# Kernel tuning notes

Measured on AMD Instinct MI355X. Metric: run time of the kernel, lower is better.

The kernel has to match this reference:

```python
import jax, jax.numpy as jnp
import numpy as np

N_NODES = 100000
N_EDGES = 1600000
D = 128
N_GRAPHS = 128
N_LAYERS = 3


def setup_inputs() -> dict:
    key = jax.random.key(0)
    ks = jax.random.split(key, 3 + 4 * N_LAYERS)
    x = jax.random.normal(ks[0], (N_NODES, D), dtype=jnp.float32)
    edge_index = jax.random.randint(ks[1], (2, N_EDGES), 0, N_NODES, dtype=jnp.int64)
    batch = jnp.sort(jax.random.randint(ks[2], (N_NODES,), 0, N_GRAPHS, dtype=jnp.int64))
    inp = {"x": x, "edge_index": edge_index, "batch": batch}
    scale = 1.0 / np.sqrt(D)
    for l in range(N_LAYERS):
        inp[f"W1_{l}"] = jax.random.normal(ks[3 + 4 * l], (D, D), dtype=jnp.float32) * scale
        inp[f"b1_{l}"] = jnp.zeros((D,), dtype=jnp.float32)
        inp[f"W2_{l}"] = jax.random.normal(ks[4 + 4 * l], (D, D), dtype=jnp.float32) * scale
        inp[f"b2_{l}"] = jnp.zeros((D,), dtype=jnp.float32)
    return inp


def _gin_conv(x, edge_index, W1, b1, W2, b2):
    # GINConv with eps=0: out = MLP(x + sum_{j in N(i)} x_j)
    msgs = x[edge_index[0]]                                   # [E, D] gather
    agg = jax.ops.segment_sum(msgs, edge_index[1], num_segments=N_NODES)
    h = x + agg
    h = jax.nn.relu(h @ W1 + b1)
    return h @ W2 + b2


def reference(x, edge_index, batch,
              W1_0, b1_0, W2_0, b2_0,
              W1_1, b1_1, W2_1, b2_1,
              W1_2, b1_2, W2_2, b2_2):
    params = [(W1_0, b1_0, W2_0, b2_0), (W1_1, b1_1, W2_1, b2_1), (W1_2, b1_2, W2_2, b2_2)]
    h = x
    for l in range(N_LAYERS - 1):
        h = _gin_conv(h, edge_index, *params[l])
        h = jax.nn.relu(h)  # act; dropout with drop_ratio=0 is identity
    node_emb = _gin_conv(h, edge_index, *params[-1])  # JK='last'
    # global_mean_pool
    sums = jax.ops.segment_sum(node_emb, batch, num_segments=N_GRAPHS)
    counts = jax.ops.segment_sum(jnp.ones((N_NODES, 1), node_emb.dtype), batch, num_segments=N_GRAPHS)
    graph_emb = sums / jnp.maximum(counts, 1.0)
    return graph_emb
```

## Files before the change

kernel.cpp:

```cpp
#include <hip/hip_runtime.h>
#include <hip/hip_bf16.h>

#define N_NODES 100000
#define N_PAD   100032
#define N_EDGES 1600000
#define DIM 128
#define N_GRAPHS 128
#define NBKT 98
#define BSTRIDE 18432
#define TILES (N_PAD / 16)
#define GRID_FUSED 1563
#define POOL_BLKS ((N_NODES + 127) / 128)
#define B1_BATCH 4096
#define B1_GRID ((N_EDGES + B1_BATCH - 1) / B1_BATCH)

typedef unsigned short u16;
typedef unsigned int u32;
typedef __attribute__((ext_vector_type(8))) short bf16x8;
typedef __attribute__((ext_vector_type(8))) unsigned short u16x8;
typedef __attribute__((ext_vector_type(4))) float f32x4;

#define MFMA(A, B, C) __builtin_amdgcn_mfma_f32_16x16x32_bf16(A, B, C, 0, 0, 0)

__device__ __forceinline__ u16 f2bf(float x) {
    u32 u = __float_as_uint(x);
    u = (u + 0x7FFFu + ((u >> 16) & 1u)) >> 16;
    return (u16)u;
}
__device__ __forceinline__ float bf2f(u16 u) {
    return __uint_as_float(((u32)u) << 16);
}

__global__ __launch_bounds__(256) void bucket1_kernel(const int* __restrict__ src,
                                                      const int* __restrict__ dst,
                                                      u32* __restrict__ cursorB,
                                                      u32* __restrict__ pairs) {
    __shared__ int lh[NBKT];
    __shared__ u32 lbase[NBKT];
    int t = threadIdx.x;
    if (t < NBKT) lh[t] = 0;
    __syncthreads();
    int e0 = blockIdx.x * B1_BATCH;
    int d[16], s[16], rk[16];
#pragma unroll
    for (int k = 0; k < 16; ++k) {
        int e = e0 + t + k * 256;
        if (e < N_EDGES) {
            d[k] = dst[e];
            s[k] = src[e];
            rk[k] = atomicAdd(&lh[d[k] >> 10], 1);
        }
    }
    __syncthreads();
    if (t < NBKT) lbase[t] = atomicAdd(&cursorB[t], (u32)lh[t]) + (u32)(t * BSTRIDE);
    __syncthreads();
#pragma unroll
    for (int k = 0; k < 16; ++k) {
        int e = e0 + t + k * 256;
        if (e < N_EDGES) {
            u32 pos = lbase[d[k] >> 10] + (u32)rk[k];
            pairs[pos] = ((u32)(d[k] & 1023) << 22) | (u32)s[k];
        }
    }
}

__global__ __launch_bounds__(1024) void bucket2_kernel(const u32* __restrict__ cursorB,
                                                       const u32* __restrict__ pairs,
                                                       int* __restrict__ row_ptr,
                                                       int* __restrict__ csr) {
    __shared__ int lh[1024];
    __shared__ int rc[1024];
    __shared__ int bs[128];
    int b = blockIdx.x, t = threadIdx.x;

    if (t < 128) bs[t] = (t < NBKT) ? (int)cursorB[t] : 0;
    __syncthreads();
    for (int off = 1; off < 128; off <<= 1) {
        int v = (t < 128 && t >= off) ? bs[t - off] : 0;
        __syncthreads();
        if (t < 128) bs[t] += v;
        __syncthreads();
    }
    int cnt = (int)cursorB[b];
    int bbase = (b == 0) ? 0 : bs[b - 1];

    lh[t] = 0;
    __syncthreads();
    const u32* pb = pairs + (size_t)b * BSTRIDE;
    for (int i = t; i < cnt; i += 1024) atomicAdd(&lh[__builtin_nontemporal_load(pb + i) >> 22], 1);
    __syncthreads();

    int own = lh[t];
    for (int off = 1; off < 1024; off <<= 1) {
        int v = (t >= off) ? lh[t - off] : 0;
        __syncthreads();
        lh[t] += v;
        __syncthreads();
    }
    int excl = lh[t] - own;
    int node = b * 1024 + t;
    if (node < N_NODES) row_ptr[node] = bbase + excl;
    if (b == 0 && t == 0) row_ptr[N_NODES] = N_EDGES;
    rc[t] = bbase + excl;
    __syncthreads();

    for (int i = t; i < cnt; i += 1024) {
        u32 p = __builtin_nontemporal_load(pb + i);
        int pos = atomicAdd(&rc[p >> 22], 1);
        csr[pos] = (int)(p & 0x3FFFFFu);
    }
}

__global__ __launch_bounds__(256) void xprep_kernel(const float* __restrict__ x,
                                                    u16* __restrict__ hb) {
    int i = blockIdx.x * 256 + threadIdx.x;
    if (i < N_NODES * 32) {
        float4 v = ((const float4*)x)[i];
        ushort4 o;
        o.x = f2bf(v.x); o.y = f2bf(v.y); o.z = f2bf(v.z); o.w = f2bf(v.w);
        ((ushort4*)hb)[i] = o;
    }
}

struct WPrepArgs {
    const float* w[6];
    u16* buf[6];
};
__global__ __launch_bounds__(256) void wprep_kernel(WPrepArgs p) {
    int m = blockIdx.y;
    int idx = blockIdx.x * 256 + threadIdx.x;
    int n = idx >> 7, k = idx & 127;
    float v = p.w[m][k * 128 + n];
    u16 hi = f2bf(v);
    p.buf[m][idx] = hi;
    p.buf[m][idx + 16384] = f2bf(v - bf2f(hi));
}

#define HS 136
__global__ __launch_bounds__(256, 2) void gin_layer(const u16* __restrict__ hin,
                                                    const int* __restrict__ rp,
                                                    const int* __restrict__ csr,
                                                    const u16* __restrict__ W1,
                                                    const float* __restrict__ b1,
                                                    const u16* __restrict__ W2,
                                                    const float* __restrict__ b2,
                                                    u16* __restrict__ hout, int relu) {
    __shared__ u16 Hh[64 * HS];
    __shared__ u16 Hl[64 * HS];
    int tid = threadIdx.x;
    int lane = tid & 63, wave = tid >> 6;
    int m16 = lane & 15, quad = lane >> 4;
    int colBase = wave * 32;
    int t0 = blockIdx.x * 4;
    int r0 = t0 * 16;

    {
        int qw = tid >> 4;
        int f  = tid & 15;
        int nb = r0 + qw * 4;
        const u16x8* h8 = (const u16x8*)hin;
#pragma unroll
        for (int j = 0; j < 4; ++j) {
            int n = nb + j;
            int nl = qw * 4 + j;
            float a[8];
            if (n < N_NODES) {
                u16x8 sv = h8[(size_t)n * 16 + f];
#pragma unroll
                for (int r = 0; r < 8; ++r) a[r] = bf2f(sv[r]);
                int s = rp[n], e = rp[n + 1];
                int i = s;
                for (; i + 8 <= e; i += 8) {
                    u16x8 v0 = h8[(size_t)csr[i + 0] * 16 + f];
                    u16x8 v1 = h8[(size_t)csr[i + 1] * 16 + f];
                    u16x8 v2 = h8[(size_t)csr[i + 2] * 16 + f];
                    u16x8 v3 = h8[(size_t)csr[i + 3] * 16 + f];
                    u16x8 v4 = h8[(size_t)csr[i + 4] * 16 + f];
                    u16x8 v5 = h8[(size_t)csr[i + 5] * 16 + f];
                    u16x8 v6 = h8[(size_t)csr[i + 6] * 16 + f];
                    u16x8 v7 = h8[(size_t)csr[i + 7] * 16 + f];
#pragma unroll
                    for (int r = 0; r < 8; ++r)
                        a[r] += ((bf2f(v0[r]) + bf2f(v1[r])) + (bf2f(v2[r]) + bf2f(v3[r]))) +
                                ((bf2f(v4[r]) + bf2f(v5[r])) + (bf2f(v6[r]) + bf2f(v7[r])));
                }
                for (; i < e; ++i) {
                    u16x8 v = h8[(size_t)csr[i] * 16 + f];
#pragma unroll
                    for (int r = 0; r < 8; ++r) a[r] += bf2f(v[r]);
                }
            } else {
#pragma unroll
                for (int r = 0; r < 8; ++r) a[r] = 0.f;
            }
            u16x8 o;
#pragma unroll
            for (int r = 0; r < 8; ++r) o[r] = f2bf(a[r]);
            *(u16x8*)&Hh[nl * HS + f * 8] = o;
        }
    }
    __syncthreads();

    bf16x8 aH[4][4];
#pragma unroll
    for (int p = 0; p < 4; ++p)
#pragma unroll
        for (int kb = 0; kb < 4; ++kb)
            aH[p][kb] = *(const bf16x8*)&Hh[(p * 16 + m16) * HS + kb * 32 + quad * 8];
    __syncthreads();

    float b1v[2][4], b2v[2][4];
#pragma unroll
    for (int nt = 0; nt < 2; ++nt)
#pragma unroll
        for (int rg = 0; rg < 4; ++rg) {
            int col = colBase + nt * 16 + quad * 4 + rg;
            b1v[nt][rg] = b1[col];
            b2v[nt][rg] = b2[col];
        }

    f32x4 z = {0.f, 0.f, 0.f, 0.f};

    bf16x8 W1H[2][4], W1L[2][4];
#pragma unroll
    for (int nt = 0; nt < 2; ++nt) {
        int n = colBase + nt * 16 + m16;
#pragma unroll
        for (int kb = 0; kb < 4; ++kb) {
            int off = n * 128 + kb * 32 + quad * 8;
            W1H[nt][kb] = *(const bf16x8*)(W1 + off);
            W1L[nt][kb] = *(const bf16x8*)(W1 + off + 16384);
        }
    }

    f32x4 acc[4][2];
#pragma unroll
    for (int p = 0; p < 4; ++p) { acc[p][0] = z; acc[p][1] = z; }

#pragma unroll
    for (int kb = 0; kb < 4; ++kb) {
#pragma unroll
        for (int p = 0; p < 4; ++p) {
            acc[p][0] = MFMA(W1H[0][kb], aH[p][kb], acc[p][0]);
            acc[p][1] = MFMA(W1H[1][kb], aH[p][kb], acc[p][1]);
            acc[p][0] = MFMA(W1L[0][kb], aH[p][kb], acc[p][0]);
            acc[p][1] = MFMA(W1L[1][kb], aH[p][kb], acc[p][1]);
        }
    }

#pragma unroll
    for (int p = 0; p < 4; ++p) {
#pragma unroll
        for (int nt = 0; nt < 2; ++nt) {
            ushort4 hv, lv;
#pragma unroll
            for (int rg = 0; rg < 4; ++rg) {
                float v = fmaxf(acc[p][nt][rg] + b1v[nt][rg], 0.f);
                u16 hi = f2bf(v);
                ((u16*)&hv)[rg] = hi;
                ((u16*)&lv)[rg] = f2bf(v - bf2f(hi));
            }
            int off = (p * 16 + m16) * HS + colBase + nt * 16 + quad * 4;
            *(ushort4*)&Hh[off] = hv;
            *(ushort4*)&Hl[off] = lv;
        }
    }
    __syncthreads();

    bf16x8 W2H[2][4], W2L[2][4];
#pragma unroll
    for (int nt = 0; nt < 2; ++nt) {
        int n = colBase + nt * 16 + m16;
#pragma unroll
        for (int kb = 0; kb < 4; ++kb) {
            int off = n * 128 + kb * 32 + quad * 8;
            W2H[nt][kb] = *(const bf16x8*)(W2 + off);
            W2L[nt][kb] = *(const bf16x8*)(W2 + off + 16384);
        }
    }

    f32x4 acc2[4][2];
#pragma unroll
    for (int p = 0; p < 4; ++p) { acc2[p][0] = z; acc2[p][1] = z; }
#pragma unroll
    for (int kb = 0; kb < 4; ++kb) {
#pragma unroll
        for (int p = 0; p < 4; ++p) {
            int off = (p * 16 + m16) * HS + kb * 32 + quad * 8;
            bf16x8 hH = *(const bf16x8*)(&Hh[off]);
            bf16x8 hL = *(const bf16x8*)(&Hl[off]);
            acc2[p][0] = MFMA(W2H[0][kb], hH, acc2[p][0]);
            acc2[p][1] = MFMA(W2H[1][kb], hH, acc2[p][1]);
            acc2[p][0] = MFMA(W2H[0][kb], hL, acc2[p][0]);
            acc2[p][1] = MFMA(W2H[1][kb], hL, acc2[p][1]);
            acc2[p][0] = MFMA(W2L[0][kb], hH, acc2[p][0]);
            acc2[p][1] = MFMA(W2L[1][kb], hH, acc2[p][1]);
        }
    }

#pragma unroll
    for (int p = 0; p < 4; ++p) {
        size_t row = (size_t)(t0 + p) * 16 + m16;
#pragma unroll
        for (int nt = 0; nt < 2; ++nt) {
            int col = colBase + nt * 16 + quad * 4;
            ushort4 o;
#pragma unroll
            for (int rg = 0; rg < 4; ++rg) {
                float v = acc2[p][nt][rg] + b2v[nt][rg];
                if (relu) v = fmaxf(v, 0.f);
                ((u16*)&o)[rg] = f2bf(v);
            }
            *(ushort4*)(hout + row * 128 + col) = o;
        }
    }
}

__global__ __launch_bounds__(256) void psum_kernel(const u16* __restrict__ h,
                                                   const int* __restrict__ batch,
                                                   float* __restrict__ sums) {
    __shared__ int sBatch[128];
    int blk = blockIdx.x, t = threadIdx.x;
    int n0 = blk * 128;
    int nEnd = min(n0 + 128, N_NODES);
    if (t < 128 && n0 + t < N_NODES) sBatch[t] = batch[n0 + t];
    __syncthreads();

    int j = t & 127;
    int half = t >> 7;
    int s = n0 + half * 64;
    int e = min(s + 64, nEnd);

    float acc = 0.f;
    int cur = -1;
    for (int n = s; n < e; ++n) {
        int g = sBatch[n - n0];
        if (g != cur) {
            if (cur >= 0) atomicAdd(&sums[cur * 128 + j], acc);
            cur = g;
            acc = 0.f;
        }
        acc += bf2f(h[(size_t)n * 128 + j]);
    }
    if (cur >= 0) atomicAdd(&sums[cur * 128 + j], acc);
}

__global__ __launch_bounds__(128) void pdiv_kernel(const float* __restrict__ sums,
                                                   const int* __restrict__ batch,
                                                   float* __restrict__ out) {
    __shared__ int sB[2];
    int g = blockIdx.x;
    if (threadIdx.x < 2) {
        int target = g + threadIdx.x;
        int lo = 0, hi = N_NODES;
        while (lo < hi) {
            int m = (lo + hi) >> 1;
            if (batch[m] < target) lo = m + 1; else hi = m;
        }
        sB[threadIdx.x] = lo;
    }
    __syncthreads();
    float cnt = (float)(sB[1] - sB[0]);
    out[g * 128 + threadIdx.x] = sums[g * 128 + threadIdx.x] / fmaxf(cnt, 1.f);
}

extern "C" void kernel_launch(void* const* d_in, const int* in_sizes, int n_in,
                              void* d_out, int out_size, void* d_ws, size_t ws_size,
                              hipStream_t stream) {
    const float* x     = (const float*)d_in[0];
    const int*   ei    = (const int*)d_in[1];
    const int*   batch = (const int*)d_in[2];
    const int*   eSrc  = ei;
    const int*   eDst  = ei + N_EDGES;

    const float* W1[3] = {(const float*)d_in[3], (const float*)d_in[7],  (const float*)d_in[11]};
    const float* b1[3] = {(const float*)d_in[4], (const float*)d_in[8],  (const float*)d_in[12]};
    const float* W2[3] = {(const float*)d_in[5], (const float*)d_in[9],  (const float*)d_in[13]};
    const float* b2[3] = {(const float*)d_in[6], (const float*)d_in[10], (const float*)d_in[14]};

    float* P2 = (float*)d_ws;
    u16*   planeB = (u16*)P2;
    u16*   planeA = (u16*)(P2 + (size_t)N_PAD * DIM);
    u16*   Ah = planeA + (size_t)N_PAD * DIM;
    u16*   Wb = Ah + (size_t)N_PAD * DIM;
    int*   row_ptr = (int*)(Wb + 6 * 32768);
    u32*   cursorB = (u32*)(row_ptr + N_NODES + 8);
    int*   csr     = (int*)(cursorB + 128);
    float* sums    = (float*)(csr + N_EDGES);
    u32*   pairs   = (u32*)P2;

    hipMemsetAsync(cursorB, 0, 128 * sizeof(u32), stream);
    bucket1_kernel<<<B1_GRID, 256, 0, stream>>>(eSrc, eDst, cursorB, pairs);
    bucket2_kernel<<<NBKT, 1024, 0, stream>>>(cursorB, pairs, row_ptr, csr);

    xprep_kernel<<<(N_NODES * 32 + 255) / 256, 256, 0, stream>>>(x, planeA);
    WPrepArgs wp;
    for (int l = 0; l < 3; ++l) {
        wp.w[2 * l]       = W1[l];
        wp.w[2 * l + 1]   = W2[l];
        wp.buf[2 * l]     = Wb + (size_t)(2 * l) * 32768;
        wp.buf[2 * l + 1] = Wb + (size_t)(2 * l + 1) * 32768;
    }
    wprep_kernel<<<dim3(64, 6), 256, 0, stream>>>(wp);
    hipMemsetAsync(sums, 0, N_GRAPHS * DIM * sizeof(float), stream);

    u16* hin  = planeA;
    u16* hout = planeB;
    for (int l = 0; l < 3; ++l) {
        gin_layer<<<GRID_FUSED, 256, 0, stream>>>(hin, row_ptr, csr,
                                                  Wb + (size_t)(2 * l) * 32768, b1[l],
                                                  Wb + (size_t)(2 * l + 1) * 32768, b2[l],
                                                  hout, (l < 2) ? 1 : 0);
        u16* tmp = hin; hin = hout; hout = tmp;
    }
    psum_kernel<<<POOL_BLKS, 256, 0, stream>>>(hin, batch, sums);
    pdiv_kernel<<<N_GRAPHS, 128, 0, stream>>>(sums, batch, (float*)d_out);
}
```

Before: 487.0 us.

## Halve gin_layer tile to 32 rows, raise occupancy, fuse prep kernels

Each gin_layer block now handles 32 nodes instead of 64. The grid doubles, LDS and register use per block halve, and launch bounds ask for 4 blocks per CU, so more waves are available to hide the latency of the irregular neighbor gathers. Separately, the x conversion, weight split and sums memset are merged into one launch to cut launch overhead. The cost is that each block loads the W1/W2 fragments from global memory for half as many rows, so weight traffic and load work per row doubles.

```diff
diff --git a/kernel.cpp b/kernel.cpp
--- a/kernel.cpp
+++ b/kernel.cpp
@@ -8,11 +8,13 @@
 #define N_GRAPHS 128
 #define NBKT 98
 #define BSTRIDE 18432
-#define TILES (N_PAD / 16)
-#define GRID_FUSED 1563
+#define GRID_FUSED 3126
 #define POOL_BLKS ((N_NODES + 127) / 128)
 #define B1_BATCH 4096
 #define B1_GRID ((N_EDGES + B1_BATCH - 1) / B1_BATCH)
+#define XPREP_BLKS 12500
+#define WPREP_BLKS 384
+#define SUMS_BLKS 64
 
 typedef unsigned short u16;
 typedef unsigned int u32;
@@ -111,33 +113,40 @@
     }
 }
 
-__global__ __launch_bounds__(256) void xprep_kernel(const float* __restrict__ x,
-                                                    u16* __restrict__ hb) {
-    int i = blockIdx.x * 256 + threadIdx.x;
-    if (i < N_NODES * 32) {
-        float4 v = ((const float4*)x)[i];
-        ushort4 o;
-        o.x = f2bf(v.x); o.y = f2bf(v.y); o.z = f2bf(v.z); o.w = f2bf(v.w);
-        ((ushort4*)hb)[i] = o;
-    }
-}
-
 struct WPrepArgs {
     const float* w[6];
     u16* buf[6];
 };
-__global__ __launch_bounds__(256) void wprep_kernel(WPrepArgs p) {
-    int m = blockIdx.y;
-    int idx = blockIdx.x * 256 + threadIdx.x;
-    int n = idx >> 7, k = idx & 127;
-    float v = p.w[m][k * 128 + n];
-    u16 hi = f2bf(v);
-    p.buf[m][idx] = hi;
-    p.buf[m][idx + 16384] = f2bf(v - bf2f(hi));
+__global__ __launch_bounds__(256) void prep_kernel(const float* __restrict__ x,
+                                                   u16* __restrict__ hb,
+                                                   WPrepArgs p,
+                                                   float* __restrict__ sums) {
+    int b = blockIdx.x, t = threadIdx.x;
+    if (b < XPREP_BLKS) {
+        int i = b * 256 + t;
+        if (i < N_NODES * 32) {
+            float4 v = ((const float4*)x)[i];
+            ushort4 o;
+            o.x = f2bf(v.x); o.y = f2bf(v.y); o.z = f2bf(v.z); o.w = f2bf(v.w);
+            ((ushort4*)hb)[i] = o;
+        }
+    } else if (b < XPREP_BLKS + WPREP_BLKS) {
+        int bb = b - XPREP_BLKS;
+        int m = bb >> 6;
+        int idx = (bb & 63) * 256 + t;
+        int n = idx >> 7, k = idx & 127;
+        float v = p.w[m][k * 128 + n];
+        u16 hi = f2bf(v);
+        p.buf[m][idx] = hi;
+        p.buf[m][idx + 16384] = f2bf(v - bf2f(hi));
+    } else {
+        int i = (b - XPREP_BLKS - WPREP_BLKS) * 256 + t;
+        if (i < N_GRAPHS * DIM) sums[i] = 0.f;
+    }
 }
 
 #define HS 136
-__global__ __launch_bounds__(256, 2) void gin_layer(const u16* __restrict__ hin,
+__global__ __launch_bounds__(256, 4) void gin_layer(const u16* __restrict__ hin,
                                                     const int* __restrict__ rp,
                                                     const int* __restrict__ csr,
                                                     const u16* __restrict__ W1,
@@ -145,24 +154,22 @@
                                                     const u16* __restrict__ W2,
                                                     const float* __restrict__ b2,
                                                     u16* __restrict__ hout, int relu) {
-    __shared__ u16 Hh[64 * HS];
-    __shared__ u16 Hl[64 * HS];
+    __shared__ u16 Hh[32 * HS];
+    __shared__ u16 Hl[32 * HS];
     int tid = threadIdx.x;
     int lane = tid & 63, wave = tid >> 6;
     int m16 = lane & 15, quad = lane >> 4;
     int colBase = wave * 32;
-    int t0 = blockIdx.x * 4;
-    int r0 = t0 * 16;
+    int r0 = blockIdx.x * 32;
 
     {
         int qw = tid >> 4;
         int f  = tid & 15;
-        int nb = r0 + qw * 4;
         const u16x8* h8 = (const u16x8*)hin;
 #pragma unroll
-        for (int j = 0; j < 4; ++j) {
-            int n = nb + j;
-            int nl = qw * 4 + j;
+        for (int j = 0; j < 2; ++j) {
+            int nl = qw * 2 + j;
+            int n = r0 + nl;
             float a[8];
             if (n < N_NODES) {
                 u16x8 sv = h8[(size_t)n * 16 + f];
@@ -201,9 +208,9 @@
     }
     __syncthreads();
 
-    bf16x8 aH[4][4];
-#pragma unroll
-    for (int p = 0; p < 4; ++p)
+    bf16x8 aH[2][4];
+#pragma unroll
+    for (int p = 0; p < 2; ++p)
 #pragma unroll
         for (int kb = 0; kb < 4; ++kb)
             aH[p][kb] = *(const bf16x8*)&Hh[(p * 16 + m16) * HS + kb * 32 + quad * 8];
@@ -233,14 +240,14 @@
         }
     }
 
-    f32x4 acc[4][2];
-#pragma unroll
-    for (int p = 0; p < 4; ++p) { acc[p][0] = z; acc[p][1] = z; }
+    f32x4 acc[2][2];
+#pragma unroll
+    for (int p = 0; p < 2; ++p) { acc[p][0] = z; acc[p][1] = z; }
 
 #pragma unroll
     for (int kb = 0; kb < 4; ++kb) {
 #pragma unroll
-        for (int p = 0; p < 4; ++p) {
+        for (int p = 0; p < 2; ++p) {
             acc[p][0] = MFMA(W1H[0][kb], aH[p][kb], acc[p][0]);
             acc[p][1] = MFMA(W1H[1][kb], aH[p][kb], acc[p][1]);
             acc[p][0] = MFMA(W1L[0][kb], aH[p][kb], acc[p][0]);
@@ -249,7 +256,7 @@
     }
 
 #pragma unroll
-    for (int p = 0; p < 4; ++p) {
+    for (int p = 0; p < 2; ++p) {
 #pragma unroll
         for (int nt = 0; nt < 2; ++nt) {
             ushort4 hv, lv;
@@ -279,13 +286,13 @@
         }
     }
 
-    f32x4 acc2[4][2];
-#pragma unroll
-    for (int p = 0; p < 4; ++p) { acc2[p][0] = z; acc2[p][1] = z; }
+    f32x4 acc2[2][2];
+#pragma unroll
+    for (int p = 0; p < 2; ++p) { acc2[p][0] = z; acc2[p][1] = z; }
 #pragma unroll
     for (int kb = 0; kb < 4; ++kb) {
 #pragma unroll
-        for (int p = 0; p < 4; ++p) {
+        for (int p = 0; p < 2; ++p) {
             int off = (p * 16 + m16) * HS + kb * 32 + quad * 8;
             bf16x8 hH = *(const bf16x8*)(&Hh[off]);
             bf16x8 hL = *(const bf16x8*)(&Hl[off]);
@@ -299,8 +306,8 @@
     }
 
 #pragma unroll
-    for (int p = 0; p < 4; ++p) {
-        size_t row = (size_t)(t0 + p) * 16 + m16;
+    for (int p = 0; p < 2; ++p) {
+        size_t row = (size_t)r0 + p * 16 + m16;
 #pragma unroll
         for (int nt = 0; nt < 2; ++nt) {
             int col = colBase + nt * 16 + quad * 4;
@@ -393,7 +400,6 @@
     bucket1_kernel<<<B1_GRID, 256, 0, stream>>>(eSrc, eDst, cursorB, pairs);
     bucket2_kernel<<<NBKT, 1024, 0, stream>>>(cursorB, pairs, row_ptr, csr);
 
-    xprep_kernel<<<(N_NODES * 32 + 255) / 256, 256, 0, stream>>>(x, planeA);
     WPrepArgs wp;
     for (int l = 0; l < 3; ++l) {
         wp.w[2 * l]       = W1[l];
@@ -401,8 +407,7 @@
         wp.buf[2 * l]     = Wb + (size_t)(2 * l) * 32768;
         wp.buf[2 * l + 1] = Wb + (size_t)(2 * l + 1) * 32768;
     }
-    wprep_kernel<<<dim3(64, 6), 256, 0, stream>>>(wp);
-    hipMemsetAsync(sums, 0, N_GRAPHS * DIM * sizeof(float), stream);
+    prep_kernel<<<XPREP_BLKS + WPREP_BLKS + SUMS_BLKS, 256, 0, stream>>>(x, planeA, wp, sums);
 
     u16* hin  = planeA;
     u16* hout = planeB;
```

Result: slower. 512.9 us (+5.3%).

## Split CSR bucket pass into sub-blocked count/scan/scatter and fuse prep kernels

Applied to the files above, without the earlier changes.

The single 98-block bucket2 kernel, which both counted and scattered each bucket in one block, is split into three kernels. Each bucket is divided into four sub-ranges that are counted in parallel, a scan turns the counts into per-sub-range offsets, and a scatter writes the CSR, so the pass runs on 392 blocks instead of 98. The x conversion, the weight conversion and the zeroing of the pool sums are merged into one launch. This cuts launches and uses more of the GPU during CSR construction, at the cost of two extra kernel launches, an extra read of the pairs, and workspace reused for the sub-counts.

```diff
diff --git a/kernel.cpp b/kernel.cpp
--- a/kernel.cpp
+++ b/kernel.cpp
@@ -8,11 +8,13 @@
 #define N_GRAPHS 128
 #define NBKT 98
 #define BSTRIDE 18432
-#define TILES (N_PAD / 16)
 #define GRID_FUSED 1563
 #define POOL_BLKS ((N_NODES + 127) / 128)
 #define B1_BATCH 4096
 #define B1_GRID ((N_EDGES + B1_BATCH - 1) / B1_BATCH)
+#define XPREP_BLKS 12500
+#define WPREP_BLKS 384
+#define SUMS_BLKS 64
 
 typedef unsigned short u16;
 typedef unsigned int u32;
@@ -64,12 +66,30 @@
     }
 }
 
-__global__ __launch_bounds__(1024) void bucket2_kernel(const u32* __restrict__ cursorB,
+__global__ __launch_bounds__(512) void bucket2a_kernel(const u32* __restrict__ cursorB,
                                                        const u32* __restrict__ pairs,
-                                                       int* __restrict__ row_ptr,
-                                                       int* __restrict__ csr) {
+                                                       int* __restrict__ subcnt) {
     __shared__ int lh[1024];
-    __shared__ int rc[1024];
+    int b = blockIdx.x >> 2, q = blockIdx.x & 3, t = threadIdx.x;
+    int cnt = (int)cursorB[b];
+    int s = (int)(((long long)cnt * q) >> 2);
+    int e = (int)(((long long)cnt * (q + 1)) >> 2);
+    lh[t] = 0; lh[t + 512] = 0;
+    __syncthreads();
+    const u32* pb = pairs + (size_t)b * BSTRIDE;
+    for (int i = s + t; i < e; i += 512)
+        atomicAdd(&lh[__builtin_nontemporal_load(pb + i) >> 22], 1);
+    __syncthreads();
+    int* sc = subcnt + (size_t)(b * 4 + q) * 1024;
+    sc[t] = lh[t];
+    sc[t + 512] = lh[t + 512];
+}
+
+__global__ __launch_bounds__(1024) void bucket2b_kernel(const u32* __restrict__ cursorB,
+                                                        const int* __restrict__ subcnt,
+                                                        int* __restrict__ row_ptr,
+                                                        int* __restrict__ suboff) {
+    __shared__ int lh[1024];
     __shared__ int bs[128];
     int b = blockIdx.x, t = threadIdx.x;
 
@@ -81,44 +101,49 @@
         if (t < 128) bs[t] += v;
         __syncthreads();
     }
-    int cnt = (int)cursorB[b];
     int bbase = (b == 0) ? 0 : bs[b - 1];
 
-    lh[t] = 0;
-    __syncthreads();
-    const u32* pb = pairs + (size_t)b * BSTRIDE;
-    for (int i = t; i < cnt; i += 1024) atomicAdd(&lh[__builtin_nontemporal_load(pb + i) >> 22], 1);
-    __syncthreads();
-
-    int own = lh[t];
+    const int* sc = subcnt + (size_t)b * 4 * 1024;
+    int c0 = sc[t], c1 = sc[1024 + t], c2 = sc[2048 + t], c3 = sc[3072 + t];
+    int tot = (c0 + c1) + (c2 + c3);
+
+    lh[t] = tot;
+    __syncthreads();
     for (int off = 1; off < 1024; off <<= 1) {
         int v = (t >= off) ? lh[t - off] : 0;
         __syncthreads();
         lh[t] += v;
         __syncthreads();
     }
-    int excl = lh[t] - own;
+    int base = bbase + lh[t] - tot;
     int node = b * 1024 + t;
-    if (node < N_NODES) row_ptr[node] = bbase + excl;
+    if (node < N_NODES) row_ptr[node] = base;
     if (b == 0 && t == 0) row_ptr[N_NODES] = N_EDGES;
-    rc[t] = bbase + excl;
-    __syncthreads();
-
-    for (int i = t; i < cnt; i += 1024) {
+    int* so = suboff + (size_t)b * 4 * 1024;
+    so[t]        = base;
+    so[1024 + t] = base + c0;
+    so[2048 + t] = base + c0 + c1;
+    so[3072 + t] = base + c0 + c1 + c2;
+}
+
+__global__ __launch_bounds__(512) void bucket2c_kernel(const u32* __restrict__ cursorB,
+                                                       const u32* __restrict__ pairs,
+                                                       const int* __restrict__ suboff,
+                                                       int* __restrict__ csr) {
+    __shared__ int rc[1024];
+    int b = blockIdx.x >> 2, q = blockIdx.x & 3, t = threadIdx.x;
+    int cnt = (int)cursorB[b];
+    int s = (int)(((long long)cnt * q) >> 2);
+    int e = (int)(((long long)cnt * (q + 1)) >> 2);
+    const int* so = suboff + (size_t)(b * 4 + q) * 1024;
+    rc[t] = so[t];
+    rc[t + 512] = so[t + 512];
+    __syncthreads();
+    const u32* pb = pairs + (size_t)b * BSTRIDE;
+    for (int i = s + t; i < e; i += 512) {
         u32 p = __builtin_nontemporal_load(pb + i);
         int pos = atomicAdd(&rc[p >> 22], 1);
         csr[pos] = (int)(p & 0x3FFFFFu);
-    }
-}
-
-__global__ __launch_bounds__(256) void xprep_kernel(const float* __restrict__ x,
-                                                    u16* __restrict__ hb) {
-    int i = blockIdx.x * 256 + threadIdx.x;
-    if (i < N_NODES * 32) {
-        float4 v = ((const float4*)x)[i];
-        ushort4 o;
-        o.x = f2bf(v.x); o.y = f2bf(v.y); o.z = f2bf(v.z); o.w = f2bf(v.w);
-        ((ushort4*)hb)[i] = o;
     }
 }
 
@@ -126,14 +151,32 @@
     const float* w[6];
     u16* buf[6];
 };
-__global__ __launch_bounds__(256) void wprep_kernel(WPrepArgs p) {
-    int m = blockIdx.y;
-    int idx = blockIdx.x * 256 + threadIdx.x;
-    int n = idx >> 7, k = idx & 127;
-    float v = p.w[m][k * 128 + n];
-    u16 hi = f2bf(v);
-    p.buf[m][idx] = hi;
-    p.buf[m][idx + 16384] = f2bf(v - bf2f(hi));
+__global__ __launch_bounds__(256) void prep_kernel(const float* __restrict__ x,
+                                                   u16* __restrict__ hb,
+                                                   WPrepArgs p,
+                                                   float* __restrict__ sums) {
+    int b = blockIdx.x, t = threadIdx.x;
+    if (b < XPREP_BLKS) {
+        int i = b * 256 + t;
+        if (i < N_NODES * 32) {
+            float4 v = ((const float4*)x)[i];
+            ushort4 o;
+            o.x = f2bf(v.x); o.y = f2bf(v.y); o.z = f2bf(v.z); o.w = f2bf(v.w);
+            ((ushort4*)hb)[i] = o;
+        }
+    } else if (b < XPREP_BLKS + WPREP_BLKS) {
+        int bb = b - XPREP_BLKS;
+        int m = bb >> 6;
+        int idx = (bb & 63) * 256 + t;
+        int n = idx >> 7, k = idx & 127;
+        float v = p.w[m][k * 128 + n];
+        u16 hi = f2bf(v);
+        p.buf[m][idx] = hi;
+        p.buf[m][idx + 16384] = f2bf(v - bf2f(hi));
+    } else {
+        int i = (b - XPREP_BLKS - WPREP_BLKS) * 256 + t;
+        if (i < N_GRAPHS * DIM) sums[i] = 0.f;
+    }
 }
 
 #define HS 136
@@ -388,12 +431,15 @@
     int*   csr     = (int*)(cursorB + 128);
     float* sums    = (float*)(csr + N_EDGES);
     u32*   pairs   = (u32*)P2;
+    int*   subcnt  = (int*)Ah;
+    int*   suboff  = subcnt + NBKT * 4 * 1024;
 
     hipMemsetAsync(cursorB, 0, 128 * sizeof(u32), stream);
     bucket1_kernel<<<B1_GRID, 256, 0, stream>>>(eSrc, eDst, cursorB, pairs);
-    bucket2_kernel<<<NBKT, 1024, 0, stream>>>(cursorB, pairs, row_ptr, csr);
-
-    xprep_kernel<<<(N_NODES * 32 + 255) / 256, 256, 0, stream>>>(x, planeA);
+    bucket2a_kernel<<<NBKT * 4, 512, 0, stream>>>(cursorB, pairs, subcnt);
+    bucket2b_kernel<<<NBKT, 1024, 0, stream>>>(cursorB, subcnt, row_ptr, suboff);
+    bucket2c_kernel<<<NBKT * 4, 512, 0, stream>>>(cursorB, pairs, suboff, csr);
+
     WPrepArgs wp;
     for (int l = 0; l < 3; ++l) {
         wp.w[2 * l]       = W1[l];
@@ -401,8 +447,7 @@
         wp.buf[2 * l]     = Wb + (size_t)(2 * l) * 32768;
         wp.buf[2 * l + 1] = Wb + (size_t)(2 * l + 1) * 32768;
     }
-    wprep_kernel<<<dim3(64, 6), 256, 0, stream>>>(wp);
-    hipMemsetAsync(sums, 0, N_GRAPHS * DIM * sizeof(float), stream);
+    prep_kernel<<<XPREP_BLKS + WPREP_BLKS + SUMS_BLKS, 256, 0, stream>>>(x, planeA, wp, sums);
 
     u16* hin  = planeA;
     u16* hout = planeB;
```

After: 491.2 us. Within noise of the previous version (+0.9%).
